# Optimization experiments

Measured on AMD Instinct MI355X. Metric: run time of the kernel, lower is better.

Reference implementation:

```python
import jax, jax.numpy as jnp
import numpy as np

B, S, F, H, O = 2048, 96, 32, 256, 6   # batch, seq_len, features, hidden, out_size
LA, RS, RE = 32, 0, 6                  # look_ahead, replace_start, replace_end


def setup_inputs() -> dict:
    key = jax.random.key(0)
    ks = jax.random.split(key, 7)
    sc = 1.0 / np.sqrt(H).astype(np.float32)
    nrm = lambda k, shp, s: jax.random.normal(k, shp, dtype=jnp.float32) * s
    return {
        "x": nrm(ks[0], (B, S, F), 1.0),
        "W_ih": nrm(ks[1], (4 * H, F), sc),
        "W_hh": nrm(ks[2], (4 * H, H), sc),
        "b_ih": nrm(ks[3], (4 * H,), sc),
        "b_hh": nrm(ks[4], (4 * H,), sc),
        "W_fc": nrm(ks[5], (O, H), sc),
        "b_fc": nrm(ks[6], (O,), sc),
    }


def _lstm_cell(xt, h, c, W_ih, W_hh, b_ih, b_hh):
    # gates: [B, 4H] in torch LSTMCell order (i, f, g, o)
    g = xt @ W_ih.T + b_ih + h @ W_hh.T + b_hh
    i, f, gg, o = jnp.split(g, 4, axis=-1)
    c_new = jax.nn.sigmoid(f) * c + jax.nn.sigmoid(i) * jnp.tanh(gg)
    h_new = jax.nn.sigmoid(o) * jnp.tanh(c_new)
    return h_new, c_new


def _ste(x):
    # straight-through estimator: binarize forward, identity backward
    hard = (x > 0).astype(x.dtype)
    return x + jax.lax.stop_gradient(hard - x)


def reference(x, W_ih, W_hh, b_ih, b_hh, W_fc, b_fc):
    h = jnp.zeros((B, H), x.dtype)
    c = jnp.zeros((B, H), x.dtype)

    # warm-up phase: consume the full sequence
    def step(carry, xt):
        h, c = carry
        h, c = _lstm_cell(xt, h, c, W_ih, W_hh, b_ih, b_hh)
        return (h, c), None

    (h, c), _ = jax.lax.scan(step, (h, c), jnp.swapaxes(x, 0, 1))  # [S,B,F]
    out = _ste(h) @ W_fc.T + b_fc  # [B, O]

    # look-ahead phase: feed predictions back into detached inputs x[:, t]
    x_la = jax.lax.stop_gradient(jnp.swapaxes(x[:, :LA], 0, 1))  # [LA,B,F]

    def la_step(carry, xt):
        h, c, o = carry
        xt = xt.at[:, RS:RE].set(o)  # grads flow through o, not x
        h, c = _lstm_cell(xt, h, c, W_ih, W_hh, b_ih, b_hh)
        o = _ste(h) @ W_fc.T + b_fc
        return (h, c, o), o

    _, la_outs = jax.lax.scan(la_step, (h, c, out), x_la)  # [LA,B,O]
    outputs = jnp.concatenate(
        [out[:, None, :], jnp.swapaxes(la_outs, 0, 1)], axis=1
    )  # [B, LA+1, O]
    return outputs
```

## Files before the change

### kernel.cpp

```cpp
#include <hip/hip_runtime.h>

#define Bsz 2048
#define Ssz 96
#define Fsz 32
#define Hsz 256
#define Osz 6
#define LAsz 32
#define RT 8
#define NSTEP (Ssz + LAsz)
#define NTHR 512
#define NKT 9
#define NGT 64
#define GLW 1044
#define SCL   1024.0f
#define SRES  2048.0f
#define INV_SR   4.8828125e-4f
#define INV_SR2  2.384185791015625e-7f
#define INV_SWH  9.5367431640625e-07

typedef __attribute__((ext_vector_type(8))) short    short8;
typedef __attribute__((ext_vector_type(8))) _Float16 half8;
typedef __attribute__((ext_vector_type(4))) float    f32x4;
typedef __attribute__((ext_vector_type(4))) unsigned int uint4v;

__device__ __forceinline__ half8 as_h8(uint4v v) {
    union { uint4v u; half8 h; } c; c.u = v; return c.h;
}
__device__ __forceinline__ half8 as_h8s(short8 v) {
    union { short8 s; half8 h; } c; c.s = v; return c.h;
}
#define MFMAF16(A, B, C) \
    __builtin_amdgcn_mfma_f32_16x16x32_f16(as_h8(A), as_h8s(B), (C), 0, 0, 0)

__device__ __forceinline__ unsigned short f16_rne(float f) {
    union { _Float16 h; unsigned short u; } c; c.h = (_Float16)f; return c.u;
}
__device__ __forceinline__ float f16_to_f(unsigned short u) {
    union { _Float16 h; unsigned short u; } c; c.u = u; return (float)c.h;
}

#define FIDX(kt, half, slot, elem) (((((kt) * 2 + (half)) * 64) + (slot)) * 8 + (elem))

__device__ __forceinline__ double exp_d(double x) {
    x = fmin(fmax(x, -700.0), 700.0);
    const double LOG2E = 1.4426950408889634074;
    const double LN2HI = 6.93147180369123816490e-01;
    const double LN2LO = 1.90821492927058770002e-10;
    double n = __builtin_rint(x * LOG2E);
    double r = fma(-n, LN2HI, x);
    r = fma(-n, LN2LO, r);
    double p = 2.5052108385441718775e-08;
    p = fma(p, r, 2.7557319223985890653e-07);
    p = fma(p, r, 2.7557319223985892511e-06);
    p = fma(p, r, 2.4801587301587301566e-05);
    p = fma(p, r, 1.9841269841269841253e-04);
    p = fma(p, r, 1.3888888888888889419e-03);
    p = fma(p, r, 8.3333333333333332177e-03);
    p = fma(p, r, 4.1666666666666664354e-02);
    p = fma(p, r, 1.6666666666666665741e-01);
    p = fma(p, r, 5.0e-01);
    p = fma(p, r, 1.0);
    p = fma(p, r, 1.0);
    long long bits = (long long)(1023 + (int)n) << 52;
    return p * __longlong_as_double(bits);
}
__device__ __forceinline__ double recip_d(double y) {
    double r = (double)(1.0f / (float)y);
    r = fma(fma(-y, r, 1.0), r, r);
    r = fma(fma(-y, r, 1.0), r, r);
    r = fma(fma(-y, r, 1.0), r, r);
    return r;
}
__device__ __forceinline__ double sigmoid_d(double x) { return recip_d(1.0 + exp_d(-x)); }
__device__ __forceinline__ double tanh_d(double x) {
    double ax = fabs(x);
    double t = exp_d(-2.0 * ax);
    double r = (1.0 - t) * recip_d(1.0 + t);
    return x >= 0.0 ? r : -r;
}

__global__ void pack_w(const float* __restrict__ W_ih,
                       const float* __restrict__ W_hh,
                       unsigned short* __restrict__ wfrag)
{
    int idx = blockIdx.x * 256 + threadIdx.x;
    if (idx >= NGT * NKT * 64) return;
    int L  = idx & 63;
    int tk = idx >> 6;
    int kt = tk % NKT, gt = tk / NKT;
    int gate = gt * 16 + (L & 15);
    int kg   = L >> 4;
    unsigned short* p = wfrag + (size_t)idx * 16;
    #pragma unroll
    for (int i = 0; i < 8; ++i) {
        int vk = kt * 32 + kg * 8 + i;
        float wv = (vk < Fsz) ? W_ih[(size_t)gate * Fsz + vk]
                              : W_hh[(size_t)gate * Hsz + (vk - Fsz)];
        float ws = wv * SCL;
        unsigned short w0 = f16_rne(ws);
        float r1 = ws - f16_to_f(w0);
        p[i]     = w0;
        p[8 + i] = f16_rne(r1 * SRES);
    }
}

__global__ __launch_bounds__(NTHR, 2) void lstm_persist(
    const float* __restrict__ x,
    const unsigned short* __restrict__ wfrag,
    const float* __restrict__ b_ih, const float* __restrict__ b_hh,
    const float* __restrict__ W_fc, const float* __restrict__ b_fc,
    float* __restrict__ out)
{
    __shared__ __align__(16) unsigned short xfrag[NKT * 2 * 64 * 8];
    __shared__ __align__(16) float gate_lds[RT * GLW];
    __shared__ __align__(16) float h_f32[RT * Hsz];
    __shared__ float  wfc_lds[Osz * Hsz];
    __shared__ double o_lds[RT][Osz];

    const int tid   = threadIdx.x;
    const int row0  = blockIdx.x * RT;
    const int w     = tid >> 6;
    const int l     = tid & 63;
    const int j     = (w << 5) + (l & 31);
    const int q     = l >> 5;
    const int rbase = q * 4;
    const int r16   = l & 15;
    const int kg    = l >> 4;

    for (int i = tid; i < NKT * 2 * 64 * 8; i += NTHR) xfrag[i] = 0;
    for (int i = tid; i < Osz * Hsz; i += NTHR) wfc_lds[i] = W_fc[i];

    const double bias0 = (double)b_ih[0 * Hsz + j] + (double)b_hh[0 * Hsz + j];
    const double bias1 = (double)b_ih[1 * Hsz + j] + (double)b_hh[1 * Hsz + j];
    const double bias2 = (double)b_ih[2 * Hsz + j] + (double)b_hh[2 * Hsz + j];
    const double bias3 = (double)b_ih[3 * Hsz + j] + (double)b_hh[3 * Hsz + j];

    double c_reg[4];
    #pragma unroll
    for (int r = 0; r < 4; ++r) c_reg[r] = 0.0;

    const unsigned short* wbase = wfrag + ((size_t)(w * 8) * NKT * 64 + l) * 16;
    const int ktw = w + 1;

    __syncthreads();

    for (int t = 0; t < NSTEP; ++t) {
        if (tid < RT * Fsz) {
            int r = tid >> 5, f = tid & 31;
            int ts = (t < Ssz) ? t : (t - Ssz);
            float v;
            if (t >= Ssz && f < Osz) v = (float)o_lds[r][f];
            else v = x[((size_t)(row0 + r) * Ssz + ts) * Fsz + f];
            float vs = v * SCL;
            unsigned short u0 = f16_rne(vs);
            float r1 = vs - f16_to_f(u0);
            int slot = ((f >> 3) << 4) | r;
            xfrag[FIDX(0, 0, slot, f & 7)] = u0;
            xfrag[FIDX(0, 1, slot, f & 7)] = f16_rne(r1 * SRES);
        }
        __syncthreads();

        short8 bh[NKT], bl[NKT];
        #pragma unroll
        for (int kt = 0; kt < NKT; ++kt) {
            bh[kt] = *(const short8*)&xfrag[FIDX(kt, 0, l, 0)];
            bl[kt] = *(const short8*)&xfrag[FIDX(kt, 1, l, 0)];
        }

        #pragma unroll 1
        for (int gt = 0; gt < 8; ++gt) {
            const unsigned short* wp = wbase + (size_t)gt * (NKT * 64 * 16);
            f32x4 c0 = {0.f, 0.f, 0.f, 0.f};
            f32x4 c1 = {0.f, 0.f, 0.f, 0.f};
            f32x4 c2 = {0.f, 0.f, 0.f, 0.f};
            #pragma unroll
            for (int kt = 0; kt < NKT; ++kt) {
                const uint4v* rec = (const uint4v*)(wp + (size_t)kt * 1024);
                uint4v a0 = rec[0];
                uint4v a1 = rec[1];
                c0 = MFMAF16(a0, bh[kt], c0);
                c1 = MFMAF16(a0, bl[kt], c1);
                c1 = MFMAF16(a1, bh[kt], c1);
                c2 = MFMAF16(a1, bl[kt], c2);
            }
            if (r16 < RT) {
                f32x4 s;
                s.x = fmaf(c2.x, INV_SR2, fmaf(c1.x, INV_SR, c0.x));
                s.y = fmaf(c2.y, INV_SR2, fmaf(c1.y, INV_SR, c0.y));
                s.z = fmaf(c2.z, INV_SR2, fmaf(c1.z, INV_SR, c0.z));
                s.w = fmaf(c2.w, INV_SR2, fmaf(c1.w, INV_SR, c0.w));
                *(f32x4*)&gate_lds[r16 * GLW + ((w * 8 + gt) << 4) + (kg << 2)] = s;
            }
        }
        __syncthreads();

        float gv0[4], gv1[4], gv2[4], gv3[4];
        #pragma unroll
        for (int rr = 0; rr < 4; ++rr) {
            int rowb = (rbase + rr) * GLW;
            gv0[rr] = gate_lds[rowb + 0 * Hsz + j];
            gv1[rr] = gate_lds[rowb + 1 * Hsz + j];
            gv2[rr] = gate_lds[rowb + 2 * Hsz + j];
            gv3[rr] = gate_lds[rowb + 3 * Hsz + j];
        }
        #pragma unroll
        for (int rr = 0; rr < 4; ++rr) {
            double t0 = bias0 + (double)gv0[rr] * INV_SWH;
            double t1 = bias1 + (double)gv1[rr] * INV_SWH;
            double t2 = bias2 + (double)gv2[rr] * INV_SWH;
            double t3 = bias3 + (double)gv3[rr] * INV_SWH;
            double si = sigmoid_d(t0);
            double sf = sigmoid_d(t1);
            double tg = tanh_d(t2);
            double so = sigmoid_d(t3);
            double cn = fma(sf, c_reg[rr], si * tg);
            c_reg[rr] = cn;
            float hf = (float)(so * tanh_d(cn));
            int row = rbase + rr;
            int i32 = j & 31;
            int slot = ((i32 >> 3) << 4) | row;
            float hs = hf * SCL;
            unsigned short u0 = f16_rne(hs);
            float r1 = hs - f16_to_f(u0);
            xfrag[FIDX(ktw, 0, slot, i32 & 7)] = u0;
            xfrag[FIDX(ktw, 1, slot, i32 & 7)] = f16_rne(r1 * SRES);
            if (t >= Ssz - 1) h_f32[row * Hsz + j] = hf;
        }

        if (t >= Ssz - 1) {
            __syncthreads();
            double a0 = 0.0, a1 = 0.0, a2 = 0.0, a3 = 0.0, a4 = 0.0, a5 = 0.0;
            #pragma unroll
            for (int m = 0; m < 4; ++m) {
                int k = l + 64 * m;
                float hv = h_f32[w * Hsz + k];
                bool b = hv > 0.0f;
                a0 += b ? (double)wfc_lds[0 * Hsz + k] : 0.0;
                a1 += b ? (double)wfc_lds[1 * Hsz + k] : 0.0;
                a2 += b ? (double)wfc_lds[2 * Hsz + k] : 0.0;
                a3 += b ? (double)wfc_lds[3 * Hsz + k] : 0.0;
                a4 += b ? (double)wfc_lds[4 * Hsz + k] : 0.0;
                a5 += b ? (double)wfc_lds[5 * Hsz + k] : 0.0;
            }
            #pragma unroll
            for (int off = 32; off >= 1; off >>= 1) {
                a0 += __shfl_down(a0, off, 64);
                a1 += __shfl_down(a1, off, 64);
                a2 += __shfl_down(a2, off, 64);
                a3 += __shfl_down(a3, off, 64);
                a4 += __shfl_down(a4, off, 64);
                a5 += __shfl_down(a5, off, 64);
            }
            if (l == 0) {
                size_t base = ((size_t)(row0 + w) * (LAsz + 1) + (t - (Ssz - 1))) * Osz;
                double o;
                o = (double)b_fc[0] + a0; o_lds[w][0] = o; out[base + 0] = (float)o;
                o = (double)b_fc[1] + a1; o_lds[w][1] = o; out[base + 1] = (float)o;
                o = (double)b_fc[2] + a2; o_lds[w][2] = o; out[base + 2] = (float)o;
                o = (double)b_fc[3] + a3; o_lds[w][3] = o; out[base + 3] = (float)o;
                o = (double)b_fc[4] + a4; o_lds[w][4] = o; out[base + 4] = (float)o;
                o = (double)b_fc[5] + a5; o_lds[w][5] = o; out[base + 5] = (float)o;
            }
            __syncthreads();
        }
    }
}

extern "C" void kernel_launch(void* const* d_in, const int* in_sizes, int n_in,
                              void* d_out, int out_size, void* d_ws, size_t ws_size,
                              hipStream_t stream)
{
    const float* x    = (const float*)d_in[0];
    const float* W_ih = (const float*)d_in[1];
    const float* W_hh = (const float*)d_in[2];
    const float* b_ih = (const float*)d_in[3];
    const float* b_hh = (const float*)d_in[4];
    const float* W_fc = (const float*)d_in[5];
    const float* b_fc = (const float*)d_in[6];
    float* out = (float*)d_out;

    unsigned short* wfrag = (unsigned short*)d_ws;

    pack_w<<<dim3((NGT * NKT * 64 + 255) / 256), dim3(256), 0, stream>>>(
        W_ih, W_hh, wfrag);

    lstm_persist<<<dim3(Bsz / RT), dim3(NTHR), 0, stream>>>(
        x, wfrag, b_ih, b_hh, W_fc, b_fc, out);
}
```

Before: 1.893 ms.

## Software-pipeline weight loads, use LDS-only barriers, feed outputs via wave shuffles

Weight fragments for the gate GEMM are now double-buffered in registers: the loads for gate tile gt+2 are issued while tile gt runs its MFMAs, and the first two tiles are preloaded before the time loop. Full __syncthreads barriers are replaced by an lgkmcnt-only wait plus s_barrier, so pending global loads no longer stall the barrier. The predicted outputs that feed the next step are broadcast inside each wave with shuffles instead of going through LDS, which removes one barrier per look-ahead step. The two middle accumulators are split to shorten the MFMA dependency chain, and the low-half activations are read from LDS inside the loop to save registers. The cost is much higher register pressure from four 9-entry uint4 arrays, which risks spills or lower occupancy.

```diff
diff --git a/kernel.cpp b/kernel.cpp
--- a/kernel.cpp
+++ b/kernel.cpp
@@ -37,6 +37,12 @@
 }
 __device__ __forceinline__ float f16_to_f(unsigned short u) {
     union { _Float16 h; unsigned short u; } c; c.u = u; return (float)c.h;
+}
+
+__device__ __forceinline__ void lgkm_barrier() {
+    asm volatile("s_waitcnt lgkmcnt(0)" ::: "memory");
+    __builtin_amdgcn_s_barrier();
+    asm volatile("" ::: "memory");
 }
 
 #define FIDX(kt, half, slot, elem) (((((kt) * 2 + (half)) * 64) + (slot)) * 8 + (elem))
@@ -104,6 +110,41 @@
     }
 }
 
+#define LOADGT(D0, D1, gtid)                                                  \
+    do {                                                                      \
+        _Pragma("unroll")                                                     \
+        for (int kt = 0; kt < NKT; ++kt) {                                    \
+            const uint4v* rp =                                                \
+                (const uint4v*)(wb8 + ((size_t)((gtid) * NKT + kt)) * 2048);  \
+            D0[kt] = rp[0];                                                   \
+            D1[kt] = rp[1];                                                   \
+        }                                                                     \
+    } while (0)
+
+#define GEMMGT(S0, S1, gtid)                                                  \
+    do {                                                                      \
+        f32x4 c0  = {0.f, 0.f, 0.f, 0.f};                                     \
+        f32x4 c1a = {0.f, 0.f, 0.f, 0.f};                                     \
+        f32x4 c1b = {0.f, 0.f, 0.f, 0.f};                                     \
+        f32x4 c2  = {0.f, 0.f, 0.f, 0.f};                                     \
+        _Pragma("unroll")                                                     \
+        for (int kt = 0; kt < NKT; ++kt) {                                    \
+            short8 blk = *(const short8*)&xfrag[FIDX(kt, 1, l, 0)];           \
+            c0  = MFMAF16(S0[kt], bh[kt], c0);                                \
+            c1a = MFMAF16(S0[kt], blk, c1a);                                  \
+            c1b = MFMAF16(S1[kt], bh[kt], c1b);                               \
+            c2  = MFMAF16(S1[kt], blk, c2);                                   \
+        }                                                                     \
+        if (r16 < RT) {                                                       \
+            f32x4 s;                                                          \
+            s.x = fmaf(c2.x, INV_SR2, fmaf(c1a.x + c1b.x, INV_SR, c0.x));     \
+            s.y = fmaf(c2.y, INV_SR2, fmaf(c1a.y + c1b.y, INV_SR, c0.y));     \
+            s.z = fmaf(c2.z, INV_SR2, fmaf(c1a.z + c1b.z, INV_SR, c0.z));     \
+            s.w = fmaf(c2.w, INV_SR2, fmaf(c1a.w + c1b.w, INV_SR, c0.w));     \
+            *(f32x4*)&gate_lds[r16 * GLW + ((w * 8 + (gtid)) << 4) + (kg << 2)] = s; \
+        }                                                                     \
+    } while (0)
+
 __global__ __launch_bounds__(NTHR, 2) void lstm_persist(
     const float* __restrict__ x,
     const unsigned short* __restrict__ wfrag,
@@ -115,7 +156,6 @@
     __shared__ __align__(16) float gate_lds[RT * GLW];
     __shared__ __align__(16) float h_f32[RT * Hsz];
     __shared__ float  wfc_lds[Osz * Hsz];
-    __shared__ double o_lds[RT][Osz];
 
     const int tid   = threadIdx.x;
     const int row0  = blockIdx.x * RT;
@@ -139,60 +179,47 @@
     #pragma unroll
     for (int r = 0; r < 4; ++r) c_reg[r] = 0.0;
 
-    const unsigned short* wbase = wfrag + ((size_t)(w * 8) * NKT * 64 + l) * 16;
+    const char* wb8 = (const char*)wfrag + ((size_t)(w * 8) * NKT * 64 + l) * 32;
     const int ktw = w + 1;
 
+    float ofeed = 0.0f;
+
+    uint4v A0[NKT], A1[NKT], C0[NKT], C1[NKT];
+    LOADGT(A0, A1, 0);
+    LOADGT(C0, C1, 1);
+
     __syncthreads();
 
     for (int t = 0; t < NSTEP; ++t) {
-        if (tid < RT * Fsz) {
-            int r = tid >> 5, f = tid & 31;
+        if (l < 32) {
+            int f = l;
             int ts = (t < Ssz) ? t : (t - Ssz);
             float v;
-            if (t >= Ssz && f < Osz) v = (float)o_lds[r][f];
-            else v = x[((size_t)(row0 + r) * Ssz + ts) * Fsz + f];
+            if (t >= Ssz && f < Osz) v = ofeed;
+            else v = x[((size_t)(row0 + w) * Ssz + ts) * Fsz + f];
             float vs = v * SCL;
             unsigned short u0 = f16_rne(vs);
             float r1 = vs - f16_to_f(u0);
-            int slot = ((f >> 3) << 4) | r;
+            int slot = ((f >> 3) << 4) | w;
             xfrag[FIDX(0, 0, slot, f & 7)] = u0;
             xfrag[FIDX(0, 1, slot, f & 7)] = f16_rne(r1 * SRES);
         }
-        __syncthreads();
-
-        short8 bh[NKT], bl[NKT];
+        lgkm_barrier();
+
+        short8 bh[NKT];
         #pragma unroll
-        for (int kt = 0; kt < NKT; ++kt) {
+        for (int kt = 0; kt < NKT; ++kt)
             bh[kt] = *(const short8*)&xfrag[FIDX(kt, 0, l, 0)];
-            bl[kt] = *(const short8*)&xfrag[FIDX(kt, 1, l, 0)];
-        }
-
-        #pragma unroll 1
-        for (int gt = 0; gt < 8; ++gt) {
-            const unsigned short* wp = wbase + (size_t)gt * (NKT * 64 * 16);
-            f32x4 c0 = {0.f, 0.f, 0.f, 0.f};
-            f32x4 c1 = {0.f, 0.f, 0.f, 0.f};
-            f32x4 c2 = {0.f, 0.f, 0.f, 0.f};
-            #pragma unroll
-            for (int kt = 0; kt < NKT; ++kt) {
-                const uint4v* rec = (const uint4v*)(wp + (size_t)kt * 1024);
-                uint4v a0 = rec[0];
-                uint4v a1 = rec[1];
-                c0 = MFMAF16(a0, bh[kt], c0);
-                c1 = MFMAF16(a0, bl[kt], c1);
-                c1 = MFMAF16(a1, bh[kt], c1);
-                c2 = MFMAF16(a1, bl[kt], c2);
-            }
-            if (r16 < RT) {
-                f32x4 s;
-                s.x = fmaf(c2.x, INV_SR2, fmaf(c1.x, INV_SR, c0.x));
-                s.y = fmaf(c2.y, INV_SR2, fmaf(c1.y, INV_SR, c0.y));
-                s.z = fmaf(c2.z, INV_SR2, fmaf(c1.z, INV_SR, c0.z));
-                s.w = fmaf(c2.w, INV_SR2, fmaf(c1.w, INV_SR, c0.w));
-                *(f32x4*)&gate_lds[r16 * GLW + ((w * 8 + gt) << 4) + (kg << 2)] = s;
-            }
-        }
-        __syncthreads();
+
+        GEMMGT(A0, A1, 0);  LOADGT(A0, A1, 2);
+        GEMMGT(C0, C1, 1);  LOADGT(C0, C1, 3);
+        GEMMGT(A0, A1, 2);  LOADGT(A0, A1, 4);
+        GEMMGT(C0, C1, 3);  LOADGT(C0, C1, 5);
+        GEMMGT(A0, A1, 4);  LOADGT(A0, A1, 6);
+        GEMMGT(C0, C1, 5);  LOADGT(C0, C1, 7);
+        GEMMGT(A0, A1, 6);  LOADGT(A0, A1, 0);
+        GEMMGT(C0, C1, 7);  LOADGT(C0, C1, 1);
+        lgkm_barrier();
 
         float gv0[4], gv1[4], gv2[4], gv3[4];
         #pragma unroll
@@ -228,7 +255,7 @@
         }
 
         if (t >= Ssz - 1) {
-            __syncthreads();
+            lgkm_barrier();
             double a0 = 0.0, a1 = 0.0, a2 = 0.0, a3 = 0.0, a4 = 0.0, a5 = 0.0;
             #pragma unroll
             for (int m = 0; m < 4; ++m) {
@@ -251,17 +278,29 @@
                 a4 += __shfl_down(a4, off, 64);
                 a5 += __shfl_down(a5, off, 64);
             }
+            double o0 = (double)b_fc[0] + a0;
+            double o1 = (double)b_fc[1] + a1;
+            double o2 = (double)b_fc[2] + a2;
+            double o3 = (double)b_fc[3] + a3;
+            double o4 = (double)b_fc[4] + a4;
+            double o5 = (double)b_fc[5] + a5;
             if (l == 0) {
                 size_t base = ((size_t)(row0 + w) * (LAsz + 1) + (t - (Ssz - 1))) * Osz;
-                double o;
-                o = (double)b_fc[0] + a0; o_lds[w][0] = o; out[base + 0] = (float)o;
-                o = (double)b_fc[1] + a1; o_lds[w][1] = o; out[base + 1] = (float)o;
-                o = (double)b_fc[2] + a2; o_lds[w][2] = o; out[base + 2] = (float)o;
-                o = (double)b_fc[3] + a3; o_lds[w][3] = o; out[base + 3] = (float)o;
-                o = (double)b_fc[4] + a4; o_lds[w][4] = o; out[base + 4] = (float)o;
-                o = (double)b_fc[5] + a5; o_lds[w][5] = o; out[base + 5] = (float)o;
+                out[base + 0] = (float)o0;
+                out[base + 1] = (float)o1;
+                out[base + 2] = (float)o2;
+                out[base + 3] = (float)o3;
+                out[base + 4] = (float)o4;
+                out[base + 5] = (float)o5;
             }
-            __syncthreads();
+            double b0 = __shfl(o0, 0, 64);
+            double b1 = __shfl(o1, 0, 64);
+            double b2 = __shfl(o2, 0, 64);
+            double b3 = __shfl(o3, 0, 64);
+            double b4 = __shfl(o4, 0, 64);
+            double b5 = __shfl(o5, 0, 64);
+            ofeed = (float)((l == 0) ? b0 : (l == 1) ? b1 : (l == 2) ? b2 :
+                            (l == 3) ? b3 : (l == 4) ? b4 : (l == 5) ? b5 : 0.0);
         }
     }
 }
```

Result: slower. 6.103 ms (+222.4%).
